# Performance work log

Hardware: AMD Instinct MI355X
Metric: run time of the kernel (lower is better)

Reference implementation:

```python
import jax, jax.numpy as jnp
import numpy as np

R = 2.0            # distance exponent
Q = 1.0            # activation exponent
SPECIFICITY = 1.0  # c in exp(-c * dist)
BETA = 3.0         # lateral competition exponent
TEMP_COMP = 1.0    # ClusterCompetition temperature
TEMP_WTA = 0.1     # SoftWTA temperature
PHI = 1.5          # association scaling
NEG_INF = -1e30

B, C, D = 1024, 512, 256


def setup_inputs() -> dict:
    key = jax.random.key(0)
    k1, k2, k3, k4, k5 = jax.random.split(key, 5)
    inp = jax.random.normal(k1, (B, D), dtype=jnp.float32)
    w_dist = jax.random.normal(k2, (C, D), dtype=jnp.float32)      # cluster centers
    attn = jax.random.uniform(k3, (D,), dtype=jnp.float32)         # dim-wise attention (>=0)
    w_assoc = jax.random.normal(k4, (C, 2), dtype=jnp.float32)     # association weights
    mask = jax.random.randint(k5, (C,), 0, 2, dtype=jnp.int32)     # recruited-cluster mask
    return {"inp": inp, "w_dist": w_dist, "attn": attn, "w_assoc": w_assoc, "mask": mask}


def reference(inp, w_dist, attn, w_assoc, mask):
    m = mask.astype(inp.dtype)                       # [C] 0/1 recruited gate
    # Distance: per-dim |x - w|^r for every (item, cluster) pair -> [B, C, D]
    dim_dist = jnp.abs(inp[:, None, :] - w_dist[None, :, :]) ** R
    # DimWiseAttention: sum-to-one constrained attention over dims
    a = attn / jnp.sum(attn)
    # ClusterActivation: H_j = exp(-c * (sum_d a_d * dist_d)^(q/r)) -> [B, C]
    wdist = jnp.einsum('bcd,d->bc', dim_dist, a)
    H = jnp.exp(-SPECIFICITY * wdist ** (Q / R))
    clusters_actv = H * m                            # MaskNonRecruit
    nonzero = m > 0
    # ClusterCompetition: softmax over recruited clusters of actv^beta (temp-scaled),
    # re-weighting each cluster's own activation.
    comp_logits = jnp.where(nonzero, BETA * jnp.log(H) / TEMP_COMP, NEG_INF)
    p_comp = jax.nn.softmax(comp_logits, axis=-1)
    competed = p_comp * clusters_actv                # [B, C]
    # SoftWTA: plain temperature softmax over recruited clusters, same re-weighting.
    wta_logits = jnp.where(nonzero, competed / TEMP_WTA, NEG_INF)
    p_wta = jax.nn.softmax(wta_logits, axis=-1)
    softwta = p_wta * competed                       # [B, C]
    # Classification: Phi-scaled linear readout to 2 classes.
    y_pred = PHI * (softwta @ w_assoc)               # [B, 2]
    return y_pred
```

## Files before the change

kernel.cpp:

```cpp
#include <hip/hip_runtime.h>
#include <math.h>

#define BN 1024
#define CN 512
#define DN 256
#define NZ 4
#define KZ (DN / NZ)
#define TM 64
#define TN 64

__launch_bounds__(256, 2)
__global__ void dist_kernel(const float* __restrict__ inp, const float* __restrict__ wd,
                            const float* __restrict__ attn, float* __restrict__ pdot) {
    __shared__ __align__(16) float aR[TM * KZ];
    __shared__ __align__(16) float bR[TN * KZ];
    __shared__ __align__(16) float s_lds[KZ];
    __shared__ float red[4];

    const int tid = threadIdx.x;
    const int m0 = blockIdx.x * TM;
    const int n0 = blockIdx.y * TN;
    const int z  = blockIdx.z;
    const int k0 = z * KZ;

    float av = attn[tid];
    float xs = av;
    #pragma unroll
    for (int off = 32; off > 0; off >>= 1) xs += __shfl_xor(xs, off);
    if ((tid & 63) == 0) red[tid >> 6] = xs;
    __syncthreads();
    const float total = red[0] + red[1] + red[2] + red[3];
    if ((tid >> 6) == z) s_lds[tid & 63] = sqrtf(av / total);
    __syncthreads();

    {
        const int k4   = tid & 15;
        const int rbase = tid >> 4;
        const float4 sv = *(const float4*)&s_lds[k4 * 4];
        #pragma unroll
        for (int p = 0; p < 4; ++p) {
            const int row = rbase + 16 * p;
            const int wi  = row * KZ + 4 * (k4 ^ (row >> 2));
            float4 a4 = *(const float4*)&inp[(m0 + row) * DN + k0 + 4 * k4];
            a4.x *= sv.x; a4.y *= sv.y; a4.z *= sv.z; a4.w *= sv.w;
            *(float4*)&aR[wi] = a4;
            float4 b4 = *(const float4*)&wd[(n0 + row) * DN + k0 + 4 * k4];
            b4.x *= sv.x; b4.y *= sv.y; b4.z *= sv.z; b4.w *= sv.w;
            *(float4*)&bR[wi] = b4;
        }
    }
    __syncthreads();

    const int tr = tid & 15;
    const int tc = tid >> 4;
    float acc[4][4] = {};

    #pragma unroll 4
    for (int k4 = 0; k4 < 16; ++k4) {
        float4 a[4], b[4];
        const int ka = 4 * (k4 ^ tr);
        const int kb = 4 * (k4 ^ tc);
        #pragma unroll
        for (int i = 0; i < 4; ++i) a[i] = *(const float4*)&aR[(4 * tr + i) * KZ + ka];
        #pragma unroll
        for (int j = 0; j < 4; ++j) b[j] = *(const float4*)&bR[(4 * tc + j) * KZ + kb];
        const float* af = (const float*)a;
        const float* bf = (const float*)b;
        #pragma unroll
        for (int kk = 0; kk < 4; ++kk)
            #pragma unroll
            for (int i = 0; i < 4; ++i) {
                const float ai = af[i * 4 + kk];
                #pragma unroll
                for (int j = 0; j < 4; ++j) {
                    const float d = ai - bf[j * 4 + kk];
                    acc[i][j] = fmaf(d, d, acc[i][j]);
                }
            }
    }

    float* po = pdot + (size_t)z * BN * CN;
    #pragma unroll
    for (int i = 0; i < 4; ++i) {
        const int r = m0 + 4 * tr + i;
        float4 o = {acc[i][0], acc[i][1], acc[i][2], acc[i][3]};
        *(float4*)&po[r * CN + n0 + 4 * tc] = o;
    }
}

#define NEG_INF_F (-1e30f)

__device__ __forceinline__ float waveMax(float v) {
    #pragma unroll
    for (int off = 32; off > 0; off >>= 1) v = fmaxf(v, __shfl_xor(v, off));
    return v;
}
__device__ __forceinline__ float waveSum(float v) {
    #pragma unroll
    for (int off = 32; off > 0; off >>= 1) v += __shfl_xor(v, off);
    return v;
}

__launch_bounds__(256, 2)
__global__ void finish_kernel(const float* __restrict__ pdot, const int* __restrict__ mask,
                              const float* __restrict__ w_assoc, float* __restrict__ y) {
    const int tid  = threadIdx.x;
    const int lane = tid & 63;
    const int b    = blockIdx.x * 4 + (tid >> 6);
    const int cb   = lane * 8;

    float t[8];
    #pragma unroll
    for (int q = 0; q < 2; ++q) {
        float4 p = {0.f, 0.f, 0.f, 0.f};
        #pragma unroll
        for (int z = 0; z < 4; ++z) {
            const float4 v = *(const float4*)&pdot[(size_t)z * BN * CN + b * CN + cb + 4 * q];
            p.x += v.x; p.y += v.y; p.z += v.z; p.w += v.w;
        }
        t[4 * q + 0] = sqrtf(p.x); t[4 * q + 1] = sqrtf(p.y);
        t[4 * q + 2] = sqrtf(p.z); t[4 * q + 3] = sqrtf(p.w);
    }

    const int4 m0 = *(const int4*)&mask[cb];
    const int4 m1 = *(const int4*)&mask[cb + 4];
    bool rec[8] = {m0.x > 0, m0.y > 0, m0.z > 0, m0.w > 0,
                   m1.x > 0, m1.y > 0, m1.z > 0, m1.w > 0};

    float l1[8], lmax = NEG_INF_F;
    #pragma unroll
    for (int j = 0; j < 8; ++j) { l1[j] = rec[j] ? (-3.0f * t[j]) : NEG_INF_F; lmax = fmaxf(lmax, l1[j]); }
    const float mx1 = waveMax(lmax);
    float e1[8], lsum = 0.f;
    #pragma unroll
    for (int j = 0; j < 8; ++j) { e1[j] = rec[j] ? expf(l1[j] - mx1) : 0.f; lsum += e1[j]; }
    const float s1 = waveSum(lsum);
    const float inv_s1 = 1.0f / s1;

    float competed[8];
    #pragma unroll
    for (int j = 0; j < 8; ++j) competed[j] = e1[j] * inv_s1 * expf(-t[j]);

    float l2[8]; lmax = NEG_INF_F;
    #pragma unroll
    for (int j = 0; j < 8; ++j) { l2[j] = rec[j] ? (competed[j] * 10.0f) : NEG_INF_F; lmax = fmaxf(lmax, l2[j]); }
    const float mx2 = waveMax(lmax);
    float e2[8]; lsum = 0.f;
    #pragma unroll
    for (int j = 0; j < 8; ++j) { e2[j] = rec[j] ? expf(l2[j] - mx2) : 0.f; lsum += e2[j]; }
    const float s2 = waveSum(lsum);
    const float inv_s2 = 1.0f / s2;

    float y0 = 0.f, y1 = 0.f;
    #pragma unroll
    for (int q = 0; q < 4; ++q) {
        const float4 wa = *(const float4*)&w_assoc[2 * cb + 4 * q];
        const float sw0 = e2[2 * q + 0] * inv_s2 * competed[2 * q + 0];
        const float sw1 = e2[2 * q + 1] * inv_s2 * competed[2 * q + 1];
        y0 = fmaf(sw0, wa.x, y0); y1 = fmaf(sw0, wa.y, y1);
        y0 = fmaf(sw1, wa.z, y0); y1 = fmaf(sw1, wa.w, y1);
    }
    y0 = waveSum(y0);
    y1 = waveSum(y1);
    if (lane == 0) {
        float2 o = {1.5f * y0, 1.5f * y1};
        *(float2*)&y[b * 2] = o;
    }
}

extern "C" void kernel_launch(void* const* d_in, const int* in_sizes, int n_in,
                              void* d_out, int out_size, void* d_ws, size_t ws_size,
                              hipStream_t stream) {
    const float* inp     = (const float*)d_in[0];
    const float* w_dist  = (const float*)d_in[1];
    const float* attn    = (const float*)d_in[2];
    const float* w_assoc = (const float*)d_in[3];
    const int*   mask    = (const int*)d_in[4];
    float* out = (float*)d_out;

    float* pdot = (float*)d_ws;

    dim3 gA(BN / TM, CN / TN, NZ);
    dist_kernel<<<gA, 256, 0, stream>>>(inp, w_dist, attn, pdot);
    finish_kernel<<<BN / 4, 256, 0, stream>>>(pdot, mask, w_assoc, out);
}
```

Baseline: 75.59 us.

## Expand weighted squared distance into norms minus dot product with prep kernel

Rewrites the attention-weighted squared distance as r_b + q_c - 2·dot, so the inner loop becomes a pure FMA dot product instead of subtract-then-FMA. A new prep kernel normalises the attention, writes the attention-scaled input, and computes per-row and per-cluster weighted squared norms. The finish kernel rebuilds the distance with a clamp at zero. Tiling also changes to 128x64 tiles with K split into 8 slices of 32. That doubles the partial-sum buffer written and read back, adds a third launch, and risks cancellation error in the expanded form.

```diff
diff --git a/kernel.cpp b/kernel.cpp
--- a/kernel.cpp
+++ b/kernel.cpp
@@ -4,87 +4,122 @@
 #define BN 1024
 #define CN 512
 #define DN 256
-#define NZ 4
-#define KZ (DN / NZ)
-#define TM 64
+#define TM 128
 #define TN 64
+#define KZ 32
+#define NZ (DN / KZ)
+
+#define XS_OFF 0
+#define R_OFF  (BN * DN)
+#define Q_OFF  (R_OFF + BN)
+#define PD_OFF (Q_OFF + CN)
+
+__launch_bounds__(256, 4)
+__global__ void prep_kernel(const float* __restrict__ inp, const float* __restrict__ wd,
+                            const float* __restrict__ attn, float* __restrict__ ws) {
+    __shared__ float red[4];
+    float* xs = ws + XS_OFF;
+    float* r  = ws + R_OFF;
+    float* q  = ws + Q_OFF;
+
+    const int tid  = threadIdx.x;
+    const int lane = tid & 63;
+    const int blk  = blockIdx.x;
+
+    float av = attn[tid];
+    float s = av;
+    #pragma unroll
+    for (int off = 32; off > 0; off >>= 1) s += __shfl_xor(s, off);
+    if (lane == 0) red[tid >> 6] = s;
+    __syncthreads();
+    const float a = av / (red[0] + red[1] + red[2] + red[3]);
+
+    float c;
+    if (blk < BN) {
+        const float x = inp[blk * DN + tid];
+        xs[blk * DN + tid] = a * x;
+        c = a * x * x;
+    } else {
+        const float w = wd[(blk - BN) * DN + tid];
+        c = a * w * w;
+    }
+    #pragma unroll
+    for (int off = 32; off > 0; off >>= 1) c += __shfl_xor(c, off);
+    __syncthreads();
+    if (lane == 0) red[tid >> 6] = c;
+    __syncthreads();
+    if (tid == 0) {
+        const float tot = red[0] + red[1] + red[2] + red[3];
+        if (blk < BN) r[blk] = tot; else q[blk - BN] = tot;
+    }
+}
 
 __launch_bounds__(256, 2)
-__global__ void dist_kernel(const float* __restrict__ inp, const float* __restrict__ wd,
-                            const float* __restrict__ attn, float* __restrict__ pdot) {
-    __shared__ __align__(16) float aR[TM * KZ];
-    __shared__ __align__(16) float bR[TN * KZ];
-    __shared__ __align__(16) float s_lds[KZ];
-    __shared__ float red[4];
+__global__ void dist_kernel(const float* __restrict__ ws_ro, const float* __restrict__ wd,
+                            float* __restrict__ ws) {
+    __shared__ __align__(16) float aT[TM * KZ];
+    __shared__ __align__(16) float bT[TN * KZ];
+
+    const float* xs = ws_ro + XS_OFF;
+    float* pdot = ws + PD_OFF + (size_t)blockIdx.z * BN * CN;
 
     const int tid = threadIdx.x;
     const int m0 = blockIdx.x * TM;
     const int n0 = blockIdx.y * TN;
-    const int z  = blockIdx.z;
-    const int k0 = z * KZ;
-
-    float av = attn[tid];
-    float xs = av;
-    #pragma unroll
-    for (int off = 32; off > 0; off >>= 1) xs += __shfl_xor(xs, off);
-    if ((tid & 63) == 0) red[tid >> 6] = xs;
-    __syncthreads();
-    const float total = red[0] + red[1] + red[2] + red[3];
-    if ((tid >> 6) == z) s_lds[tid & 63] = sqrtf(av / total);
-    __syncthreads();
+    const int k0 = blockIdx.z * KZ;
 
     {
-        const int k4   = tid & 15;
-        const int rbase = tid >> 4;
-        const float4 sv = *(const float4*)&s_lds[k4 * 4];
-        #pragma unroll
-        for (int p = 0; p < 4; ++p) {
-            const int row = rbase + 16 * p;
-            const int wi  = row * KZ + 4 * (k4 ^ (row >> 2));
-            float4 a4 = *(const float4*)&inp[(m0 + row) * DN + k0 + 4 * k4];
-            a4.x *= sv.x; a4.y *= sv.y; a4.z *= sv.z; a4.w *= sv.w;
-            *(float4*)&aR[wi] = a4;
-            float4 b4 = *(const float4*)&wd[(n0 + row) * DN + k0 + 4 * k4];
-            b4.x *= sv.x; b4.y *= sv.y; b4.z *= sv.z; b4.w *= sv.w;
-            *(float4*)&bR[wi] = b4;
-        }
+        const int row = tid >> 1;
+        const int g0  = (tid & 1) * 4;
+        const int sw  = (row >> 3) & 7;
+        const float* src = &xs[(m0 + row) * DN + k0 + 4 * g0];
+        float4* dst = (float4*)&aT[row * KZ];
+        #pragma unroll
+        for (int j = 0; j < 4; ++j)
+            dst[(g0 + j) ^ sw] = *(const float4*)&src[4 * j];
+    }
+    {
+        const int row = tid >> 2;
+        const int g0  = (tid & 3) * 2;
+        const int sw  = (row >> 3) & 7;
+        const float* src = &wd[(n0 + row) * DN + k0 + 4 * g0];
+        float4* dst = (float4*)&bT[row * KZ];
+        #pragma unroll
+        for (int j = 0; j < 2; ++j)
+            dst[(g0 + j) ^ sw] = *(const float4*)&src[4 * j];
     }
     __syncthreads();
 
     const int tr = tid & 15;
     const int tc = tid >> 4;
-    float acc[4][4] = {};
-
-    #pragma unroll 4
-    for (int k4 = 0; k4 < 16; ++k4) {
-        float4 a[4], b[4];
-        const int ka = 4 * (k4 ^ tr);
-        const int kb = 4 * (k4 ^ tc);
-        #pragma unroll
-        for (int i = 0; i < 4; ++i) a[i] = *(const float4*)&aR[(4 * tr + i) * KZ + ka];
-        #pragma unroll
-        for (int j = 0; j < 4; ++j) b[j] = *(const float4*)&bR[(4 * tc + j) * KZ + kb];
-        const float* af = (const float*)a;
-        const float* bf = (const float*)b;
-        #pragma unroll
-        for (int kk = 0; kk < 4; ++kk)
+    const int swa = tr & 7;
+    const int swb = (tc >> 1) & 7;
+    float acc[8][4] = {};
+
+    #pragma unroll
+    for (int k4 = 0; k4 < KZ / 4; ++k4) {
+        float4 av[8], bv[4];
+        #pragma unroll
+        for (int i = 0; i < 8; ++i)
+            av[i] = ((const float4*)&aT[(8 * tr + i) * KZ])[k4 ^ swa];
+        #pragma unroll
+        for (int j = 0; j < 4; ++j)
+            bv[j] = ((const float4*)&bT[(4 * tc + j) * KZ])[k4 ^ swb];
+        #pragma unroll
+        for (int i = 0; i < 8; ++i)
             #pragma unroll
-            for (int i = 0; i < 4; ++i) {
-                const float ai = af[i * 4 + kk];
-                #pragma unroll
-                for (int j = 0; j < 4; ++j) {
-                    const float d = ai - bf[j * 4 + kk];
-                    acc[i][j] = fmaf(d, d, acc[i][j]);
-                }
+            for (int j = 0; j < 4; ++j) {
+                float t = fmaf(av[i].x, bv[j].x, acc[i][j]);
+                t = fmaf(av[i].y, bv[j].y, t);
+                t = fmaf(av[i].z, bv[j].z, t);
+                acc[i][j] = fmaf(av[i].w, bv[j].w, t);
             }
     }
 
-    float* po = pdot + (size_t)z * BN * CN;
-    #pragma unroll
-    for (int i = 0; i < 4; ++i) {
-        const int r = m0 + 4 * tr + i;
+    #pragma unroll
+    for (int i = 0; i < 8; ++i) {
         float4 o = {acc[i][0], acc[i][1], acc[i][2], acc[i][3]};
-        *(float4*)&po[r * CN + n0 + 4 * tc] = o;
+        *(float4*)&pdot[(m0 + 8 * tr + i) * CN + n0 + 4 * tc] = o;
     }
 }
 
@@ -102,30 +137,42 @@
 }
 
 __launch_bounds__(256, 2)
-__global__ void finish_kernel(const float* __restrict__ pdot, const int* __restrict__ mask,
+__global__ void finish_kernel(const float* __restrict__ ws, const int* __restrict__ mask,
                               const float* __restrict__ w_assoc, float* __restrict__ y) {
+    const float* r    = ws + R_OFF;
+    const float* q    = ws + Q_OFF;
+    const float* pdot = ws + PD_OFF;
+
     const int tid  = threadIdx.x;
     const int lane = tid & 63;
     const int b    = blockIdx.x * 4 + (tid >> 6);
     const int cb   = lane * 8;
 
+    float dot[8] = {};
+    #pragma unroll
+    for (int z = 0; z < NZ; ++z) {
+        const float* pz = &pdot[(size_t)z * BN * CN + b * CN + cb];
+        #pragma unroll
+        for (int s4 = 0; s4 < 2; ++s4) {
+            const float4 v = *(const float4*)&pz[4 * s4];
+            dot[4 * s4 + 0] += v.x; dot[4 * s4 + 1] += v.y;
+            dot[4 * s4 + 2] += v.z; dot[4 * s4 + 3] += v.w;
+        }
+    }
+    const float rb = r[b];
+    const float4 q0 = *(const float4*)&q[cb];
+    const float4 q1 = *(const float4*)&q[cb + 4];
+    const float qv[8] = {q0.x, q0.y, q0.z, q0.w, q1.x, q1.y, q1.z, q1.w};
+
     float t[8];
     #pragma unroll
-    for (int q = 0; q < 2; ++q) {
-        float4 p = {0.f, 0.f, 0.f, 0.f};
-        #pragma unroll
-        for (int z = 0; z < 4; ++z) {
-            const float4 v = *(const float4*)&pdot[(size_t)z * BN * CN + b * CN + cb + 4 * q];
-            p.x += v.x; p.y += v.y; p.z += v.z; p.w += v.w;
-        }
-        t[4 * q + 0] = sqrtf(p.x); t[4 * q + 1] = sqrtf(p.y);
-        t[4 * q + 2] = sqrtf(p.z); t[4 * q + 3] = sqrtf(p.w);
-    }
-
-    const int4 m0 = *(const int4*)&mask[cb];
-    const int4 m1 = *(const int4*)&mask[cb + 4];
-    bool rec[8] = {m0.x > 0, m0.y > 0, m0.z > 0, m0.w > 0,
-                   m1.x > 0, m1.y > 0, m1.z > 0, m1.w > 0};
+    for (int j = 0; j < 8; ++j)
+        t[j] = sqrtf(fmaxf(rb + qv[j] - 2.0f * dot[j], 0.0f));
+
+    const int4 mm0 = *(const int4*)&mask[cb];
+    const int4 mm1 = *(const int4*)&mask[cb + 4];
+    const bool rec[8] = {mm0.x > 0, mm0.y > 0, mm0.z > 0, mm0.w > 0,
+                         mm1.x > 0, mm1.y > 0, mm1.z > 0, mm1.w > 0};
 
     float l1[8], lmax = NEG_INF_F;
     #pragma unroll
@@ -134,8 +181,7 @@
     float e1[8], lsum = 0.f;
     #pragma unroll
     for (int j = 0; j < 8; ++j) { e1[j] = rec[j] ? expf(l1[j] - mx1) : 0.f; lsum += e1[j]; }
-    const float s1 = waveSum(lsum);
-    const float inv_s1 = 1.0f / s1;
+    const float inv_s1 = 1.0f / waveSum(lsum);
 
     float competed[8];
     #pragma unroll
@@ -148,15 +194,14 @@
     float e2[8]; lsum = 0.f;
     #pragma unroll
     for (int j = 0; j < 8; ++j) { e2[j] = rec[j] ? expf(l2[j] - mx2) : 0.f; lsum += e2[j]; }
-    const float s2 = waveSum(lsum);
-    const float inv_s2 = 1.0f / s2;
+    const float inv_s2 = 1.0f / waveSum(lsum);
 
     float y0 = 0.f, y1 = 0.f;
     #pragma unroll
-    for (int q = 0; q < 4; ++q) {
-        const float4 wa = *(const float4*)&w_assoc[2 * cb + 4 * q];
-        const float sw0 = e2[2 * q + 0] * inv_s2 * competed[2 * q + 0];
-        const float sw1 = e2[2 * q + 1] * inv_s2 * competed[2 * q + 1];
+    for (int p = 0; p < 4; ++p) {
+        const float4 wa = *(const float4*)&w_assoc[2 * cb + 4 * p];
+        const float sw0 = e2[2 * p + 0] * inv_s2 * competed[2 * p + 0];
+        const float sw1 = e2[2 * p + 1] * inv_s2 * competed[2 * p + 1];
         y0 = fmaf(sw0, wa.x, y0); y1 = fmaf(sw0, wa.y, y1);
         y0 = fmaf(sw1, wa.z, y0); y1 = fmaf(sw1, wa.w, y1);
     }
@@ -177,10 +222,10 @@
     const float* w_assoc = (const float*)d_in[3];
     const int*   mask    = (const int*)d_in[4];
     float* out = (float*)d_out;
-
-    float* pdot = (float*)d_ws;
-
+    float* ws  = (float*)d_ws;
+
+    prep_kernel<<<BN + CN, 256, 0, stream>>>(inp, w_dist, attn, ws);
     dim3 gA(BN / TM, CN / TN, NZ);
-    dist_kernel<<<gA, 256, 0, stream>>>(inp, w_dist, attn, pdot);
-    finish_kernel<<<BN / 4, 256, 0, stream>>>(pdot, mask, w_assoc, out);
-}
+    dist_kernel<<<gA, 256, 0, stream>>>(ws, w_dist, ws);
+    finish_kernel<<<BN / 4, 256, 0, stream>>>(ws, mask, w_assoc, out);
+}
```

Result: slower. 82.94 us (+9.7%).
